# Optimization experiments

Measured on AMD Instinct MI355X. Metric: run time of the kernel, lower is better.

The kernel has to match this reference:

```python
import jax, jax.numpy as jnp
import numpy as np

N_NODES = 50000


def gcn_conv(x, W, b, src, dst, num_nodes):
    # x: [N, Fin] -> lin -> [N, Fout]; gather source feats per edge, scatter-add at dst.
    h = x @ W                                   # [N, Fout]
    msg = h[src]                                # [E, Fout]  (message = x_j, no edge_weight)
    out = jax.ops.segment_sum(msg, dst, num_segments=num_nodes)  # [N, Fout]
    return out + b


def setup_inputs() -> dict:
    key = jax.random.key(0)
    k1, k2, k3, k4 = jax.random.split(key, 4)
    x = jax.random.normal(k1, (N_NODES, 128), dtype=jnp.float32)
    edge_index = jax.random.randint(k2, (2, 800000), 0, N_NODES, dtype=jnp.int64)
    W1 = jax.random.normal(k3, (128, 256), dtype=jnp.float32) * (1.0 / np.sqrt(128))
    b1 = jnp.zeros((256,), dtype=jnp.float32)
    W2 = jax.random.normal(k4, (256, 40), dtype=jnp.float32) * (1.0 / np.sqrt(256))
    b2 = jnp.zeros((40,), dtype=jnp.float32)
    return {"x": x, "edge_index": edge_index, "W1": W1, "b1": b1, "W2": W2, "b2": b2}


def reference(x, edge_index, W1, b1, W2, b2):
    src, dst = edge_index[0], edge_index[1]
    h = gcn_conv(x, W1, b1, src, dst, N_NODES)
    h = jax.nn.relu(h)
    out = gcn_conv(h, W2, b2, src, dst, N_NODES)
    return out
```

## Files before the change

### kernel.cpp

```cpp
#include <hip/hip_runtime.h>

typedef unsigned int u32;
typedef unsigned short u16;
using f32x4 = __attribute__((ext_vector_type(4))) float;
using f32x2 = __attribute__((ext_vector_type(2))) float;
using s16x8 = __attribute__((ext_vector_type(8))) short;
using s16x4 = __attribute__((ext_vector_type(4))) short;

__device__ __forceinline__ u16 rne_bf16(float f) {
  u32 u = __float_as_uint(f);
  u += 0x7FFF + ((u >> 16) & 1);
  return (u16)(u >> 16);
}
__device__ __forceinline__ float bf_lo(u32 u) { return __uint_as_float(u << 16); }
__device__ __forceinline__ float bf_hi(u32 u) { return __uint_as_float(u & 0xFFFF0000u); }

#define NBX 12500
#define CAP 64
#define SCAT 2048

__global__ void zero_k(int4* __restrict__ cnt4, int nc4) {
  int i = blockIdx.x * 256 + threadIdx.x;
  if (i < nc4) cnt4[i] = make_int4(0, 0, 0, 0);
}

__global__ __launch_bounds__(256) void mega_k(const int* __restrict__ srcv,
                                              const int* __restrict__ dstv,
                                              int* __restrict__ cnt,
                                              u16* __restrict__ adj,
                                              int E, int nbin,
                                              const float* __restrict__ x, u32* __restrict__ xb,
                                              int n2,
                                              const float* __restrict__ W1, u16* __restrict__ W1t,
                                              const float* __restrict__ W2, u16* __restrict__ W2t) {
  int b = blockIdx.x, t = threadIdx.x;
  if (b < SCAT) {
    int p = b & 7;
    int lo = p * nbin, hi = lo + nbin;
    int g = b >> 3;
    int ngroups = SCAT >> 3;
    int stride = ngroups * 256;
    for (int i = g * 256 + t; i < E; i += stride) {
      int d = dstv[i];
      if (d >= lo && d < hi) {
        int pos = atomicAdd(&cnt[d], 1);
        if (pos < CAP) adj[(size_t)d * CAP + pos] = (u16)srcv[i];
      }
    }
  } else if (b < SCAT + NBX) {
    int i = (b - SCAT) * 256 + t;
    if (i < n2) {
      f32x2 v = *((const f32x2*)x + i);
      xb[i] = (u32)rne_bf16(v.x) | ((u32)rne_bf16(v.y) << 16);
    }
  } else if (b < SCAT + NBX + 128) {
    int idx = (b - SCAT - NBX) * 256 + t;
    int n = idx >> 7, k = idx & 127;
    W1t[idx] = rne_bf16(W1[k * 256 + n]);
  } else {
    int idx = (b - SCAT - NBX - 128) * 256 + t;
    int c = idx >> 8, k = idx & 255;
    W2t[idx] = (c < 40) ? rne_bf16(W2[k * 40 + c]) : (u16)0;
  }
}

__global__ void agg128_k(const u32* __restrict__ xb, const u16* __restrict__ adj,
                         const int* __restrict__ cnt, u32* __restrict__ aggb, int n) {
  int lane = threadIdx.x & 63;
  int node = blockIdx.x * 4 + (threadIdx.x >> 6);
  if (node >= n) return;
  int deg = cnt[node]; if (deg > CAP) deg = CAP;
  const u16* ab = adj + (size_t)node * CAP;
  float ax = 0.f, ay = 0.f;
  int i = 0;
  for (; i + 8 <= deg; i += 8) {
    u32 u0 = xb[(size_t)ab[i] * 64 + lane];
    u32 u1 = xb[(size_t)ab[i + 1] * 64 + lane];
    u32 u2 = xb[(size_t)ab[i + 2] * 64 + lane];
    u32 u3 = xb[(size_t)ab[i + 3] * 64 + lane];
    u32 u4 = xb[(size_t)ab[i + 4] * 64 + lane];
    u32 u5 = xb[(size_t)ab[i + 5] * 64 + lane];
    u32 u6 = xb[(size_t)ab[i + 6] * 64 + lane];
    u32 u7 = xb[(size_t)ab[i + 7] * 64 + lane];
    ax += ((bf_lo(u0) + bf_lo(u1)) + (bf_lo(u2) + bf_lo(u3)))
        + ((bf_lo(u4) + bf_lo(u5)) + (bf_lo(u6) + bf_lo(u7)));
    ay += ((bf_hi(u0) + bf_hi(u1)) + (bf_hi(u2) + bf_hi(u3)))
        + ((bf_hi(u4) + bf_hi(u5)) + (bf_hi(u6) + bf_hi(u7)));
  }
  for (; i + 2 <= deg; i += 2) {
    u32 u0 = xb[(size_t)ab[i] * 64 + lane];
    u32 u1 = xb[(size_t)ab[i + 1] * 64 + lane];
    ax += bf_lo(u0) + bf_lo(u1); ay += bf_hi(u0) + bf_hi(u1);
  }
  for (; i < deg; ++i) {
    u32 u = xb[(size_t)ab[i] * 64 + lane];
    ax += bf_lo(u); ay += bf_hi(u);
  }
  aggb[(size_t)node * 64 + lane] = (u32)rne_bf16(ax) | ((u32)rne_bf16(ay) << 16);
}

__global__ __launch_bounds__(64) void fused_k(const u16* __restrict__ Ab,
                                              const u16* __restrict__ W1t,
                                              const float* __restrict__ b1,
                                              const u16* __restrict__ W2t,
                                              u32* __restrict__ zb, int M) {
  __shared__ short slab[2][16 * 34];
  const int l = threadIdx.x;
  const int p = l & 15, g = l >> 4;
  const int m0 = blockIdx.x * 32;

  s16x8 af[2][4];
  #pragma unroll
  for (int rt = 0; rt < 2; ++rt) {
    int mrow = m0 + rt * 16 + p;
    int mload = (mrow < M) ? mrow : (M - 1);
    const u16* arow = Ab + (size_t)mload * 128 + g * 8;
    #pragma unroll
    for (int kt = 0; kt < 4; ++kt) af[rt][kt] = *(const s16x8*)(arow + kt * 32);
  }

  f32x4 acc2[2][3];
  #pragma unroll
  for (int rt = 0; rt < 2; ++rt)
    #pragma unroll
    for (int n2 = 0; n2 < 3; ++n2) acc2[rt][n2] = (f32x4){0.f, 0.f, 0.f, 0.f};

  #pragma unroll 2
  for (int s = 0; s < 8; ++s) {
    const int n0 = 2 * s, n1 = 2 * s + 1;
    const u16* w0 = W1t + (size_t)(n0 * 16 + p) * 128 + g * 8;
    const u16* w1 = W1t + (size_t)(n1 * 16 + p) * 128 + g * 8;
    s16x8 wA[4], wB[4];
    #pragma unroll
    for (int kt = 0; kt < 4; ++kt) {
      wA[kt] = *(const s16x8*)(w0 + kt * 32);
      wB[kt] = *(const s16x8*)(w1 + kt * 32);
    }
    float4 bva = *(const float4*)(b1 + n0 * 16 + g * 4);
    float4 bvb = *(const float4*)(b1 + n1 * 16 + g * 4);
    #pragma unroll
    for (int rt = 0; rt < 2; ++rt) {
      f32x4 aA = {0.f, 0.f, 0.f, 0.f};
      f32x4 aB = {0.f, 0.f, 0.f, 0.f};
      #pragma unroll
      for (int kt = 0; kt < 4; ++kt) {
        aA = __builtin_amdgcn_mfma_f32_16x16x32_bf16(wA[kt], af[rt][kt], aA, 0, 0, 0);
        aB = __builtin_amdgcn_mfma_f32_16x16x32_bf16(wB[kt], af[rt][kt], aB, 0, 0, 0);
      }
      s16x4 pa, pb;
      pa[0] = (short)rne_bf16(fmaxf(aA[0] + bva.x, 0.f));
      pa[1] = (short)rne_bf16(fmaxf(aA[1] + bva.y, 0.f));
      pa[2] = (short)rne_bf16(fmaxf(aA[2] + bva.z, 0.f));
      pa[3] = (short)rne_bf16(fmaxf(aA[3] + bva.w, 0.f));
      pb[0] = (short)rne_bf16(fmaxf(aB[0] + bvb.x, 0.f));
      pb[1] = (short)rne_bf16(fmaxf(aB[1] + bvb.y, 0.f));
      pb[2] = (short)rne_bf16(fmaxf(aB[2] + bvb.z, 0.f));
      pb[3] = (short)rne_bf16(fmaxf(aB[3] + bvb.w, 0.f));
      *(s16x4*)&slab[rt][p * 34 + g * 4] = pa;
      *(s16x4*)&slab[rt][p * 34 + 16 + g * 4] = pb;
    }
    #pragma unroll
    for (int n2 = 0; n2 < 3; ++n2) {
      s16x8 wf = *(const s16x8*)(W2t + (size_t)(n2 * 16 + p) * 256 + s * 32 + g * 8);
      #pragma unroll
      for (int rt = 0; rt < 2; ++rt) {
        s16x8 a2 = *(const s16x8*)&slab[rt][p * 34 + g * 8];
        acc2[rt][n2] = __builtin_amdgcn_mfma_f32_16x16x32_bf16(wf, a2, acc2[rt][n2], 0, 0, 0);
      }
    }
  }

  #pragma unroll
  for (int rt = 0; rt < 2; ++rt) {
    int mrow = m0 + rt * 16 + p;
    if (mrow < M) {
      #pragma unroll
      for (int n2 = 0; n2 < 3; ++n2) {
        int c0 = n2 * 16 + g * 4;
        if (c0 < 40) {
          uint2 o;
          o.x = (u32)rne_bf16(acc2[rt][n2][0]) | ((u32)rne_bf16(acc2[rt][n2][1]) << 16);
          o.y = (u32)rne_bf16(acc2[rt][n2][2]) | ((u32)rne_bf16(acc2[rt][n2][3]) << 16);
          *(uint2*)(zb + (size_t)mrow * 20 + n2 * 8 + g * 2) = o;
        }
      }
    }
  }
}

__global__ void agg40_k(const u32* __restrict__ zb, const u16* __restrict__ adj,
                        const int* __restrict__ cnt, const float* __restrict__ bias,
                        float* __restrict__ outp, int n) {
  int hl = threadIdx.x & 31;
  int node = blockIdx.x * 8 + (threadIdx.x >> 5);
  if (node >= n || hl >= 20) return;
  int deg = cnt[node]; if (deg > CAP) deg = CAP;
  const u16* ab = adj + (size_t)node * CAP;
  float ax = 0.f, ay = 0.f;
  int i = 0;
  for (; i + 4 <= deg; i += 4) {
    u32 u0 = zb[(size_t)ab[i] * 20 + hl];
    u32 u1 = zb[(size_t)ab[i + 1] * 20 + hl];
    u32 u2 = zb[(size_t)ab[i + 2] * 20 + hl];
    u32 u3 = zb[(size_t)ab[i + 3] * 20 + hl];
    ax += (bf_lo(u0) + bf_lo(u1)) + (bf_lo(u2) + bf_lo(u3));
    ay += (bf_hi(u0) + bf_hi(u1)) + (bf_hi(u2) + bf_hi(u3));
  }
  for (; i < deg; ++i) {
    u32 u = zb[(size_t)ab[i] * 20 + hl];
    ax += bf_lo(u); ay += bf_hi(u);
  }
  float2 bv = ((const float2*)bias)[hl];
  ((float2*)(outp + (size_t)node * 40))[hl] = make_float2(ax + bv.x, ay + bv.y);
}

extern "C" void kernel_launch(void* const* d_in, const int* in_sizes, int n_in,
                              void* d_out, int out_size, void* d_ws, size_t ws_size,
                              hipStream_t stream) {
  const float* x  = (const float*)d_in[0];
  const int*   ei = (const int*)d_in[1];
  const float* W1 = (const float*)d_in[2];
  const float* b1 = (const float*)d_in[3];
  const float* W2 = (const float*)d_in[4];
  const float* b2 = (const float*)d_in[5];
  float* out = (float*)d_out;

  int N = in_sizes[0] / 128;
  int E = in_sizes[1] / 2;
  const int* src = ei;
  const int* dst = ei + E;

  char* ws = (char*)d_ws;
  size_t off = 0;
  auto carve = [&](size_t bytes) {
    char* p = ws + off;
    off += (bytes + 255) & ~(size_t)255;
    return p;
  };
  u32* xb    = (u32*)carve((size_t)N * 128 * 2);
  u32* aggb  = (u32*)carve((size_t)N * 128 * 2);
  u16* W1t   = (u16*)carve(256 * 128 * 2);
  u16* W2t   = (u16*)carve(48 * 256 * 2);
  u32* zbuf  = (u32*)carve((size_t)N * 20 * 4);
  int* cnt   = (int*)carve((size_t)N * 4);
  u16* adj   = (u16*)carve((size_t)N * CAP * 2);

  int nbin = (N + 7) / 8;
  int nc4 = (N + 3) / 4;

  zero_k<<<(nc4 + 255) / 256, 256, 0, stream>>>((int4*)cnt, nc4);
  mega_k<<<SCAT + NBX + 128 + 48, 256, 0, stream>>>(src, dst, cnt, adj, E, nbin,
                                                    x, xb, N * 64, W1, W1t, W2, W2t);
  agg128_k<<<(N + 3) / 4, 256, 0, stream>>>(xb, adj, cnt, aggb, N);
  fused_k<<<(N + 31) / 32, 64, 0, stream>>>((const u16*)aggb, W1t, b1, W2t, zbuf, N);
  agg40_k<<<(N + 7) / 8, 256, 0, stream>>>(zbuf, adj, cnt, b2, out, N);
}
```

Baseline: 128.0 us.

## Split 128-wide aggregation into feature slices and enlarge fused GEMM row tile

The first aggregation kernel now assigns 16 lanes per node and splits the 64-word feature row into four 16-word slices, each handled by its own group of blocks. The aim is a smaller gathered working set per block sweep, which should help cache locality on random neighbor gathers, at the cost of re-reading adjacency and degree four times. The fused two-layer GEMM kernel now processes 64 rows per block instead of 32 and hoists the W2 fragment loads, so weight loads are amortised over more rows. The price is higher register pressure and fewer blocks in flight.

```diff
diff --git a/kernel.cpp b/kernel.cpp
--- a/kernel.cpp
+++ b/kernel.cpp
@@ -64,54 +64,49 @@
   }
 }
 
-__global__ void agg128_k(const u32* __restrict__ xb, const u16* __restrict__ adj,
-                         const int* __restrict__ cnt, u32* __restrict__ aggb, int n) {
-  int lane = threadIdx.x & 63;
-  int node = blockIdx.x * 4 + (threadIdx.x >> 6);
+__global__ __launch_bounds__(256) void agg128_k(const u32* __restrict__ xb,
+                                                const u16* __restrict__ adj,
+                                                const int* __restrict__ cnt,
+                                                u32* __restrict__ aggb, int n, int nbp) {
+  int f = blockIdx.x / nbp;
+  int nb = blockIdx.x % nbp;
+  int sg = (threadIdx.x >> 4);
+  int s  = threadIdx.x & 15;
+  int node = nb * 16 + sg;
   if (node >= n) return;
   int deg = cnt[node]; if (deg > CAP) deg = CAP;
   const u16* ab = adj + (size_t)node * CAP;
+  const u32* base = xb + f * 16 + s;
   float ax = 0.f, ay = 0.f;
   int i = 0;
-  for (; i + 8 <= deg; i += 8) {
-    u32 u0 = xb[(size_t)ab[i] * 64 + lane];
-    u32 u1 = xb[(size_t)ab[i + 1] * 64 + lane];
-    u32 u2 = xb[(size_t)ab[i + 2] * 64 + lane];
-    u32 u3 = xb[(size_t)ab[i + 3] * 64 + lane];
-    u32 u4 = xb[(size_t)ab[i + 4] * 64 + lane];
-    u32 u5 = xb[(size_t)ab[i + 5] * 64 + lane];
-    u32 u6 = xb[(size_t)ab[i + 6] * 64 + lane];
-    u32 u7 = xb[(size_t)ab[i + 7] * 64 + lane];
-    ax += ((bf_lo(u0) + bf_lo(u1)) + (bf_lo(u2) + bf_lo(u3)))
-        + ((bf_lo(u4) + bf_lo(u5)) + (bf_lo(u6) + bf_lo(u7)));
-    ay += ((bf_hi(u0) + bf_hi(u1)) + (bf_hi(u2) + bf_hi(u3)))
-        + ((bf_hi(u4) + bf_hi(u5)) + (bf_hi(u6) + bf_hi(u7)));
-  }
-  for (; i + 2 <= deg; i += 2) {
-    u32 u0 = xb[(size_t)ab[i] * 64 + lane];
-    u32 u1 = xb[(size_t)ab[i + 1] * 64 + lane];
-    ax += bf_lo(u0) + bf_lo(u1); ay += bf_hi(u0) + bf_hi(u1);
+  for (; i + 4 <= deg; i += 4) {
+    u32 u0 = base[(size_t)ab[i] * 64];
+    u32 u1 = base[(size_t)ab[i + 1] * 64];
+    u32 u2 = base[(size_t)ab[i + 2] * 64];
+    u32 u3 = base[(size_t)ab[i + 3] * 64];
+    ax += (bf_lo(u0) + bf_lo(u1)) + (bf_lo(u2) + bf_lo(u3));
+    ay += (bf_hi(u0) + bf_hi(u1)) + (bf_hi(u2) + bf_hi(u3));
   }
   for (; i < deg; ++i) {
-    u32 u = xb[(size_t)ab[i] * 64 + lane];
+    u32 u = base[(size_t)ab[i] * 64];
     ax += bf_lo(u); ay += bf_hi(u);
   }
-  aggb[(size_t)node * 64 + lane] = (u32)rne_bf16(ax) | ((u32)rne_bf16(ay) << 16);
-}
-
-__global__ __launch_bounds__(64) void fused_k(const u16* __restrict__ Ab,
-                                              const u16* __restrict__ W1t,
-                                              const float* __restrict__ b1,
-                                              const u16* __restrict__ W2t,
-                                              u32* __restrict__ zb, int M) {
-  __shared__ short slab[2][16 * 34];
+  aggb[(size_t)node * 64 + f * 16 + s] = (u32)rne_bf16(ax) | ((u32)rne_bf16(ay) << 16);
+}
+
+__global__ __launch_bounds__(64, 1) void fused_k(const u16* __restrict__ Ab,
+                                                 const u16* __restrict__ W1t,
+                                                 const float* __restrict__ b1,
+                                                 const u16* __restrict__ W2t,
+                                                 u32* __restrict__ zb, int M) {
+  __shared__ short slab[4][16 * 34];
   const int l = threadIdx.x;
   const int p = l & 15, g = l >> 4;
-  const int m0 = blockIdx.x * 32;
-
-  s16x8 af[2][4];
+  const int m0 = blockIdx.x * 64;
+
+  s16x8 af[4][4];
   #pragma unroll
-  for (int rt = 0; rt < 2; ++rt) {
+  for (int rt = 0; rt < 4; ++rt) {
     int mrow = m0 + rt * 16 + p;
     int mload = (mrow < M) ? mrow : (M - 1);
     const u16* arow = Ab + (size_t)mload * 128 + g * 8;
@@ -119,9 +114,9 @@
     for (int kt = 0; kt < 4; ++kt) af[rt][kt] = *(const s16x8*)(arow + kt * 32);
   }
 
-  f32x4 acc2[2][3];
+  f32x4 acc2[4][3];
   #pragma unroll
-  for (int rt = 0; rt < 2; ++rt)
+  for (int rt = 0; rt < 4; ++rt)
     #pragma unroll
     for (int n2 = 0; n2 < 3; ++n2) acc2[rt][n2] = (f32x4){0.f, 0.f, 0.f, 0.f};
 
@@ -130,16 +125,19 @@
     const int n0 = 2 * s, n1 = 2 * s + 1;
     const u16* w0 = W1t + (size_t)(n0 * 16 + p) * 128 + g * 8;
     const u16* w1 = W1t + (size_t)(n1 * 16 + p) * 128 + g * 8;
-    s16x8 wA[4], wB[4];
+    s16x8 wA[4], wB[4], wf[3];
     #pragma unroll
     for (int kt = 0; kt < 4; ++kt) {
       wA[kt] = *(const s16x8*)(w0 + kt * 32);
       wB[kt] = *(const s16x8*)(w1 + kt * 32);
     }
+    #pragma unroll
+    for (int n2 = 0; n2 < 3; ++n2)
+      wf[n2] = *(const s16x8*)(W2t + (size_t)(n2 * 16 + p) * 256 + s * 32 + g * 8);
     float4 bva = *(const float4*)(b1 + n0 * 16 + g * 4);
     float4 bvb = *(const float4*)(b1 + n1 * 16 + g * 4);
     #pragma unroll
-    for (int rt = 0; rt < 2; ++rt) {
+    for (int rt = 0; rt < 4; ++rt) {
       f32x4 aA = {0.f, 0.f, 0.f, 0.f};
       f32x4 aB = {0.f, 0.f, 0.f, 0.f};
       #pragma unroll
@@ -161,17 +159,16 @@
     }
     #pragma unroll
     for (int n2 = 0; n2 < 3; ++n2) {
-      s16x8 wf = *(const s16x8*)(W2t + (size_t)(n2 * 16 + p) * 256 + s * 32 + g * 8);
       #pragma unroll
-      for (int rt = 0; rt < 2; ++rt) {
+      for (int rt = 0; rt < 4; ++rt) {
         s16x8 a2 = *(const s16x8*)&slab[rt][p * 34 + g * 8];
-        acc2[rt][n2] = __builtin_amdgcn_mfma_f32_16x16x32_bf16(wf, a2, acc2[rt][n2], 0, 0, 0);
+        acc2[rt][n2] = __builtin_amdgcn_mfma_f32_16x16x32_bf16(wf[n2], a2, acc2[rt][n2], 0, 0, 0);
       }
     }
   }
 
   #pragma unroll
-  for (int rt = 0; rt < 2; ++rt) {
+  for (int rt = 0; rt < 4; ++rt) {
     int mrow = m0 + rt * 16 + p;
     if (mrow < M) {
       #pragma unroll
@@ -247,11 +244,12 @@
 
   int nbin = (N + 7) / 8;
   int nc4 = (N + 3) / 4;
+  int nbp = (N + 15) / 16;
 
   zero_k<<<(nc4 + 255) / 256, 256, 0, stream>>>((int4*)cnt, nc4);
   mega_k<<<SCAT + NBX + 128 + 48, 256, 0, stream>>>(src, dst, cnt, adj, E, nbin,
                                                     x, xb, N * 64, W1, W1t, W2, W2t);
-  agg128_k<<<(N + 3) / 4, 256, 0, stream>>>(xb, adj, cnt, aggb, N);
-  fused_k<<<(N + 31) / 32, 64, 0, stream>>>((const u16*)aggb, W1t, b1, W2t, zbuf, N);
+  agg128_k<<<4 * nbp, 256, 0, stream>>>(xb, adj, cnt, aggb, N, nbp);
+  fused_k<<<(N + 63) / 64, 64, 0, stream>>>((const u16*)aggb, W1t, b1, W2t, zbuf, N);
   agg40_k<<<(N + 7) / 8, 256, 0, stream>>>(zbuf, adj, cnt, b2, out, N);
 }
```

After: 141.6 us. 10.6% more time.

## Fuse 128-wide neighbor aggregation into the MLP GEMM kernel via LDS tile

Applied to the files above, without the earlier changes.

The separate agg128 kernel and the global aggb buffer are removed. A new 512-thread kernel has eight waves gather and sum neighbor features for 32 nodes straight into a shared-memory tile. Wave 0 then loads its MFMA A-fragments from that tile instead of from global memory. This drops one kernel launch and the write and re-read of the aggregated intermediate. In exchange, seven of the eight waves sit idle during the GEMM phase, and the block's LDS stays occupied until wave 0 finishes, which may reduce occupancy.

```diff
diff --git a/kernel.cpp b/kernel.cpp
--- a/kernel.cpp
+++ b/kernel.cpp
@@ -64,60 +64,63 @@
   }
 }
 
-__global__ void agg128_k(const u32* __restrict__ xb, const u16* __restrict__ adj,
-                         const int* __restrict__ cnt, u32* __restrict__ aggb, int n) {
-  int lane = threadIdx.x & 63;
-  int node = blockIdx.x * 4 + (threadIdx.x >> 6);
-  if (node >= n) return;
-  int deg = cnt[node]; if (deg > CAP) deg = CAP;
-  const u16* ab = adj + (size_t)node * CAP;
-  float ax = 0.f, ay = 0.f;
-  int i = 0;
-  for (; i + 8 <= deg; i += 8) {
-    u32 u0 = xb[(size_t)ab[i] * 64 + lane];
-    u32 u1 = xb[(size_t)ab[i + 1] * 64 + lane];
-    u32 u2 = xb[(size_t)ab[i + 2] * 64 + lane];
-    u32 u3 = xb[(size_t)ab[i + 3] * 64 + lane];
-    u32 u4 = xb[(size_t)ab[i + 4] * 64 + lane];
-    u32 u5 = xb[(size_t)ab[i + 5] * 64 + lane];
-    u32 u6 = xb[(size_t)ab[i + 6] * 64 + lane];
-    u32 u7 = xb[(size_t)ab[i + 7] * 64 + lane];
-    ax += ((bf_lo(u0) + bf_lo(u1)) + (bf_lo(u2) + bf_lo(u3)))
-        + ((bf_lo(u4) + bf_lo(u5)) + (bf_lo(u6) + bf_lo(u7)));
-    ay += ((bf_hi(u0) + bf_hi(u1)) + (bf_hi(u2) + bf_hi(u3)))
-        + ((bf_hi(u4) + bf_hi(u5)) + (bf_hi(u6) + bf_hi(u7)));
-  }
-  for (; i + 2 <= deg; i += 2) {
-    u32 u0 = xb[(size_t)ab[i] * 64 + lane];
-    u32 u1 = xb[(size_t)ab[i + 1] * 64 + lane];
-    ax += bf_lo(u0) + bf_lo(u1); ay += bf_hi(u0) + bf_hi(u1);
-  }
-  for (; i < deg; ++i) {
-    u32 u = xb[(size_t)ab[i] * 64 + lane];
-    ax += bf_lo(u); ay += bf_hi(u);
-  }
-  aggb[(size_t)node * 64 + lane] = (u32)rne_bf16(ax) | ((u32)rne_bf16(ay) << 16);
-}
-
-__global__ __launch_bounds__(64) void fused_k(const u16* __restrict__ Ab,
-                                              const u16* __restrict__ W1t,
-                                              const float* __restrict__ b1,
-                                              const u16* __restrict__ W2t,
-                                              u32* __restrict__ zb, int M) {
+__global__ __launch_bounds__(512) void gfused_k(const u32* __restrict__ xb,
+                                                const u16* __restrict__ adj,
+                                                const int* __restrict__ cnt,
+                                                const u16* __restrict__ W1t,
+                                                const float* __restrict__ b1,
+                                                const u16* __restrict__ W2t,
+                                                u32* __restrict__ zb, int M) {
+  __shared__ u32 tile[32][68];
   __shared__ short slab[2][16 * 34];
-  const int l = threadIdx.x;
-  const int p = l & 15, g = l >> 4;
+  const int wid = threadIdx.x >> 6;
+  const int lane = threadIdx.x & 63;
   const int m0 = blockIdx.x * 32;
+
+  for (int q = 0; q < 4; ++q) {
+    int row = wid * 4 + q;
+    int node = m0 + row;
+    int nd = (node < M) ? node : (M - 1);
+    int deg = cnt[nd]; if (deg > CAP) deg = CAP;
+    const u16* ab = adj + (size_t)nd * CAP;
+    float ax = 0.f, ay = 0.f;
+    int i = 0;
+    for (; i + 8 <= deg; i += 8) {
+      u32 u0 = xb[(size_t)ab[i] * 64 + lane];
+      u32 u1 = xb[(size_t)ab[i + 1] * 64 + lane];
+      u32 u2 = xb[(size_t)ab[i + 2] * 64 + lane];
+      u32 u3 = xb[(size_t)ab[i + 3] * 64 + lane];
+      u32 u4 = xb[(size_t)ab[i + 4] * 64 + lane];
+      u32 u5 = xb[(size_t)ab[i + 5] * 64 + lane];
+      u32 u6 = xb[(size_t)ab[i + 6] * 64 + lane];
+      u32 u7 = xb[(size_t)ab[i + 7] * 64 + lane];
+      ax += ((bf_lo(u0) + bf_lo(u1)) + (bf_lo(u2) + bf_lo(u3)))
+          + ((bf_lo(u4) + bf_lo(u5)) + (bf_lo(u6) + bf_lo(u7)));
+      ay += ((bf_hi(u0) + bf_hi(u1)) + (bf_hi(u2) + bf_hi(u3)))
+          + ((bf_hi(u4) + bf_hi(u5)) + (bf_hi(u6) + bf_hi(u7)));
+    }
+    for (; i + 2 <= deg; i += 2) {
+      u32 u0 = xb[(size_t)ab[i] * 64 + lane];
+      u32 u1 = xb[(size_t)ab[i + 1] * 64 + lane];
+      ax += bf_lo(u0) + bf_lo(u1); ay += bf_hi(u0) + bf_hi(u1);
+    }
+    for (; i < deg; ++i) {
+      u32 u = xb[(size_t)ab[i] * 64 + lane];
+      ax += bf_lo(u); ay += bf_hi(u);
+    }
+    tile[row][lane] = (u32)rne_bf16(ax) | ((u32)rne_bf16(ay) << 16);
+  }
+  __syncthreads();
+  if (wid != 0) return;
+
+  const int p = lane & 15, g = lane >> 4;
 
   s16x8 af[2][4];
   #pragma unroll
-  for (int rt = 0; rt < 2; ++rt) {
-    int mrow = m0 + rt * 16 + p;
-    int mload = (mrow < M) ? mrow : (M - 1);
-    const u16* arow = Ab + (size_t)mload * 128 + g * 8;
-    #pragma unroll
-    for (int kt = 0; kt < 4; ++kt) af[rt][kt] = *(const s16x8*)(arow + kt * 32);
-  }
+  for (int rt = 0; rt < 2; ++rt)
+    #pragma unroll
+    for (int kt = 0; kt < 4; ++kt)
+      af[rt][kt] = *(const s16x8*)&tile[rt * 16 + p][kt * 16 + g * 4];
 
   f32x4 acc2[2][3];
   #pragma unroll
@@ -238,7 +241,6 @@
     return p;
   };
   u32* xb    = (u32*)carve((size_t)N * 128 * 2);
-  u32* aggb  = (u32*)carve((size_t)N * 128 * 2);
   u16* W1t   = (u16*)carve(256 * 128 * 2);
   u16* W2t   = (u16*)carve(48 * 256 * 2);
   u32* zbuf  = (u32*)carve((size_t)N * 20 * 4);
@@ -251,7 +253,6 @@
   zero_k<<<(nc4 + 255) / 256, 256, 0, stream>>>((int4*)cnt, nc4);
   mega_k<<<SCAT + NBX + 128 + 48, 256, 0, stream>>>(src, dst, cnt, adj, E, nbin,
                                                     x, xb, N * 64, W1, W1t, W2, W2t);
-  agg128_k<<<(N + 3) / 4, 256, 0, stream>>>(xb, adj, cnt, aggb, N);
-  fused_k<<<(N + 31) / 32, 64, 0, stream>>>((const u16*)aggb, W1t, b1, W2t, zbuf, N);
+  gfused_k<<<(N + 31) / 32, 512, 0, stream>>>(xb, adj, cnt, W1t, b1, W2t, zbuf, N);
   agg40_k<<<(N + 7) / 8, 256, 0, stream>>>(zbuf, adj, cnt, b2, out, N);
 }
```

After: 156.8 us. +22.5%, slower.

## Pack four waves per fused block and pad layer-2 rows to 32 words

Applied to the files above, without the earlier changes.

The fused two-layer MFMA kernel now runs four independent 32-row waves per 256-thread block, each with its own shared-memory slab, instead of one wave per block. The W2 fragment loads are hoisted ahead of the layer-1 MFMAs, and the loop unroll drops to 1 with an added block barrier each iteration. The intermediate z buffer row stride grows from 20 to 32 words so each gathered row is 128-byte aligned for the second aggregation. The stride change costs extra memory footprint, and the new per-iteration barrier is not needed because the slabs are per-wave, so waves may stall on each other.

```diff
diff --git a/kernel.cpp b/kernel.cpp
--- a/kernel.cpp
+++ b/kernel.cpp
@@ -18,6 +18,7 @@
 #define NBX 12500
 #define CAP 64
 #define SCAT 2048
+#define ZSTR 32
 
 __global__ void zero_k(int4* __restrict__ cnt4, int nc4) {
   int i = blockIdx.x * 256 + threadIdx.x;
@@ -99,15 +100,16 @@
   aggb[(size_t)node * 64 + lane] = (u32)rne_bf16(ax) | ((u32)rne_bf16(ay) << 16);
 }
 
-__global__ __launch_bounds__(64) void fused_k(const u16* __restrict__ Ab,
-                                              const u16* __restrict__ W1t,
-                                              const float* __restrict__ b1,
-                                              const u16* __restrict__ W2t,
-                                              u32* __restrict__ zb, int M) {
-  __shared__ short slab[2][16 * 34];
-  const int l = threadIdx.x;
+__global__ __launch_bounds__(256) void fused_k(const u16* __restrict__ Ab,
+                                               const u16* __restrict__ W1t,
+                                               const float* __restrict__ b1,
+                                               const u16* __restrict__ W2t,
+                                               u32* __restrict__ zb, int M) {
+  __shared__ short slab[4][2][16 * 34];
+  const int wid = threadIdx.x >> 6;
+  const int l = threadIdx.x & 63;
   const int p = l & 15, g = l >> 4;
-  const int m0 = blockIdx.x * 32;
+  const int m0 = (blockIdx.x * 4 + wid) * 32;
 
   s16x8 af[2][4];
   #pragma unroll
@@ -125,17 +127,21 @@
     #pragma unroll
     for (int n2 = 0; n2 < 3; ++n2) acc2[rt][n2] = (f32x4){0.f, 0.f, 0.f, 0.f};
 
-  #pragma unroll 2
+  #pragma unroll 1
   for (int s = 0; s < 8; ++s) {
+    __syncthreads();
     const int n0 = 2 * s, n1 = 2 * s + 1;
     const u16* w0 = W1t + (size_t)(n0 * 16 + p) * 128 + g * 8;
     const u16* w1 = W1t + (size_t)(n1 * 16 + p) * 128 + g * 8;
-    s16x8 wA[4], wB[4];
+    s16x8 wA[4], wB[4], wf[3];
     #pragma unroll
     for (int kt = 0; kt < 4; ++kt) {
       wA[kt] = *(const s16x8*)(w0 + kt * 32);
       wB[kt] = *(const s16x8*)(w1 + kt * 32);
     }
+    #pragma unroll
+    for (int n2 = 0; n2 < 3; ++n2)
+      wf[n2] = *(const s16x8*)(W2t + (size_t)(n2 * 16 + p) * 256 + s * 32 + g * 8);
     float4 bva = *(const float4*)(b1 + n0 * 16 + g * 4);
     float4 bvb = *(const float4*)(b1 + n1 * 16 + g * 4);
     #pragma unroll
@@ -156,16 +162,15 @@
       pb[1] = (short)rne_bf16(fmaxf(aB[1] + bvb.y, 0.f));
       pb[2] = (short)rne_bf16(fmaxf(aB[2] + bvb.z, 0.f));
       pb[3] = (short)rne_bf16(fmaxf(aB[3] + bvb.w, 0.f));
-      *(s16x4*)&slab[rt][p * 34 + g * 4] = pa;
-      *(s16x4*)&slab[rt][p * 34 + 16 + g * 4] = pb;
+      *(s16x4*)&slab[wid][rt][p * 34 + g * 4] = pa;
+      *(s16x4*)&slab[wid][rt][p * 34 + 16 + g * 4] = pb;
     }
     #pragma unroll
     for (int n2 = 0; n2 < 3; ++n2) {
-      s16x8 wf = *(const s16x8*)(W2t + (size_t)(n2 * 16 + p) * 256 + s * 32 + g * 8);
       #pragma unroll
       for (int rt = 0; rt < 2; ++rt) {
-        s16x8 a2 = *(const s16x8*)&slab[rt][p * 34 + g * 8];
-        acc2[rt][n2] = __builtin_amdgcn_mfma_f32_16x16x32_bf16(wf, a2, acc2[rt][n2], 0, 0, 0);
+        s16x8 a2 = *(const s16x8*)&slab[wid][rt][p * 34 + g * 8];
+        acc2[rt][n2] = __builtin_amdgcn_mfma_f32_16x16x32_bf16(wf[n2], a2, acc2[rt][n2], 0, 0, 0);
       }
     }
   }
@@ -181,7 +186,7 @@
           uint2 o;
           o.x = (u32)rne_bf16(acc2[rt][n2][0]) | ((u32)rne_bf16(acc2[rt][n2][1]) << 16);
           o.y = (u32)rne_bf16(acc2[rt][n2][2]) | ((u32)rne_bf16(acc2[rt][n2][3]) << 16);
-          *(uint2*)(zb + (size_t)mrow * 20 + n2 * 8 + g * 2) = o;
+          *(uint2*)(zb + (size_t)mrow * ZSTR + n2 * 8 + g * 2) = o;
         }
       }
     }
@@ -199,15 +204,15 @@
   float ax = 0.f, ay = 0.f;
   int i = 0;
   for (; i + 4 <= deg; i += 4) {
-    u32 u0 = zb[(size_t)ab[i] * 20 + hl];
-    u32 u1 = zb[(size_t)ab[i + 1] * 20 + hl];
-    u32 u2 = zb[(size_t)ab[i + 2] * 20 + hl];
-    u32 u3 = zb[(size_t)ab[i + 3] * 20 + hl];
+    u32 u0 = zb[(size_t)ab[i] * ZSTR + hl];
+    u32 u1 = zb[(size_t)ab[i + 1] * ZSTR + hl];
+    u32 u2 = zb[(size_t)ab[i + 2] * ZSTR + hl];
+    u32 u3 = zb[(size_t)ab[i + 3] * ZSTR + hl];
     ax += (bf_lo(u0) + bf_lo(u1)) + (bf_lo(u2) + bf_lo(u3));
     ay += (bf_hi(u0) + bf_hi(u1)) + (bf_hi(u2) + bf_hi(u3));
   }
   for (; i < deg; ++i) {
-    u32 u = zb[(size_t)ab[i] * 20 + hl];
+    u32 u = zb[(size_t)ab[i] * ZSTR + hl];
     ax += bf_lo(u); ay += bf_hi(u);
   }
   float2 bv = ((const float2*)bias)[hl];
@@ -241,7 +246,7 @@
   u32* aggb  = (u32*)carve((size_t)N * 128 * 2);
   u16* W1t   = (u16*)carve(256 * 128 * 2);
   u16* W2t   = (u16*)carve(48 * 256 * 2);
-  u32* zbuf  = (u32*)carve((size_t)N * 20 * 4);
+  u32* zbuf  = (u32*)carve((size_t)N * ZSTR * 4);
   int* cnt   = (int*)carve((size_t)N * 4);
   u16* adj   = (u16*)carve((size_t)N * CAP * 2);
 
@@ -252,6 +257,6 @@
   mega_k<<<SCAT + NBX + 128 + 48, 256, 0, stream>>>(src, dst, cnt, adj, E, nbin,
                                                     x, xb, N * 64, W1, W1t, W2, W2t);
   agg128_k<<<(N + 3) / 4, 256, 0, stream>>>(xb, adj, cnt, aggb, N);
-  fused_k<<<(N + 31) / 32, 64, 0, stream>>>((const u16*)aggb, W1t, b1, W2t, zbuf, N);
+  fused_k<<<(N + 127) / 128, 256, 0, stream>>>((const u16*)aggb, W1t, b1, W2t, zbuf, N);
   agg40_k<<<(N + 7) / 8, 256, 0, stream>>>(zbuf, adj, cnt, b2, out, N);
 }
```

Result: slower. 130.7 us (+2.1%).
